# Optimization experiments

Measured on AMD Instinct MI355X. Metric: run time of the kernel, lower is better.

## Reference

```python
import jax, jax.numpy as jnp
import numpy as np

DIM = 128
NUM_TILES = 50000
NUM_PIECES = 25000
E_TT = 600000
E_PT = 400000


def _mean_aggregate(msgs, dst, num_dst):
    # msgs: [E, dim], dst: [E] int -> [num_dst, dim]
    agg = jax.ops.segment_sum(msgs, dst, num_segments=num_dst)
    cnt = jax.ops.segment_sum(jnp.ones((dst.shape[0], 1), msgs.dtype), dst,
                              num_segments=num_dst)
    return agg / jnp.maximum(cnt, 1.0)


def _linear(x, W, b):
    # torch nn.Linear: y = x @ W.T + b, W: [out, in]
    return x @ W.T + b


def setup_inputs() -> dict:
    key = jax.random.key(0)
    ks = jax.random.split(key, 20)
    s = 1.0 / np.sqrt(DIM)
    s2 = 1.0 / np.sqrt(2 * DIM)
    inp = {
        "tile_h": jax.random.normal(ks[0], (NUM_TILES, DIM), jnp.float32),
        "piece_h": jax.random.normal(ks[1], (NUM_PIECES, DIM), jnp.float32),
        "tile_src": jax.random.randint(ks[2], (E_PT,), 0, NUM_TILES),
        "piece_dst": jax.random.randint(ks[3], (E_PT,), 0, NUM_PIECES),
        "piece_src": jax.random.randint(ks[4], (E_PT,), 0, NUM_PIECES),
        "tile_dst": jax.random.randint(ks[5], (E_PT,), 0, NUM_TILES),
        "t_src": jax.random.randint(ks[6], (E_TT,), 0, NUM_TILES),
        "t_dst": jax.random.randint(ks[7], (E_TT,), 0, NUM_TILES),
        # weights: torch Linear layout [out_features, in_features]
        "W_t2p": jax.random.uniform(ks[8], (DIM, DIM), jnp.float32, -s, s),
        "b_t2p": jax.random.uniform(ks[9], (DIM,), jnp.float32, -s, s),
        "W_pu": jax.random.uniform(ks[10], (DIM, 2 * DIM), jnp.float32, -s2, s2),
        "b_pu": jax.random.uniform(ks[11], (DIM,), jnp.float32, -s2, s2),
        "W_p2t": jax.random.uniform(ks[12], (DIM, DIM), jnp.float32, -s, s),
        "b_p2t": jax.random.uniform(ks[13], (DIM,), jnp.float32, -s, s),
        "W_tup": jax.random.uniform(ks[14], (DIM, 2 * DIM), jnp.float32, -s2, s2),
        "b_tup": jax.random.uniform(ks[15], (DIM,), jnp.float32, -s2, s2),
        "W_t2t": jax.random.uniform(ks[16], (DIM, DIM), jnp.float32, -s, s),
        "b_t2t": jax.random.uniform(ks[17], (DIM,), jnp.float32, -s, s),
        "W_tut": jax.random.uniform(ks[18], (DIM, 2 * DIM), jnp.float32, -s2, s2),
        "b_tut": jax.random.uniform(ks[19], (DIM,), jnp.float32, -s2, s2),
    }
    return inp


def reference(tile_h, piece_h, tile_src, piece_dst, piece_src, tile_dst,
              t_src, t_dst,
              W_t2p, b_t2p, W_pu, b_pu, W_p2t, b_p2t,
              W_tup, b_tup, W_t2t, b_t2t, W_tut, b_tut):
    num_tiles = tile_h.shape[0]
    num_pieces = piece_h.shape[0]

    # Stage 1: tile -> piece
    msgs = _linear(tile_h[tile_src], W_t2p, b_t2p)          # [E_pt, dim]
    agg = _mean_aggregate(msgs, piece_dst, num_pieces)
    piece_h = jax.nn.relu(_linear(jnp.concatenate([piece_h, agg], axis=1), W_pu, b_pu))

    # Stage 2: piece -> tile
    msgs = _linear(piece_h[piece_src], W_p2t, b_p2t)        # [E_pt, dim]
    agg = _mean_aggregate(msgs, tile_dst, num_tiles)
    tile_h = jax.nn.relu(_linear(jnp.concatenate([tile_h, agg], axis=1), W_tup, b_tup))

    # Stage 3: tile -> tile
    msgs = _linear(tile_h[t_src], W_t2t, b_t2t)             # [E_tt, dim]
    agg = _mean_aggregate(msgs, t_dst, num_tiles)
    tile_h = jax.nn.relu(_linear(jnp.concatenate([tile_h, agg], axis=1), W_tut, b_tut))

    return (tile_h, piece_h)
```

## Files before the change

### kernel.cpp

```cpp
#include <hip/hip_runtime.h>
#include <hip/hip_bf16.h>

#define DIM 128
#define EPB 4096
#define BINS 512

typedef unsigned short u16;
typedef unsigned int u32;
typedef __attribute__((ext_vector_type(8))) short v8s;
typedef __attribute__((ext_vector_type(4))) float v4f;

__device__ __forceinline__ float bf2f(u16 u) {
    union { unsigned int i; float f; } v;
    v.i = ((unsigned int)u) << 16;
    return v.f;
}

__device__ __forceinline__ u16 f2bf(float f) {
    union { float f; unsigned int i; } v;
    v.f = f;
    unsigned int x = v.i;
    return (u16)((x + 0x7fffu + ((x >> 16) & 1u)) >> 16);
}

__device__ __forceinline__ uint4 pack8(float4 x0, float4 x1) {
    uint4 o;
    o.x = (u32)f2bf(x0.x) | ((u32)f2bf(x0.y) << 16);
    o.y = (u32)f2bf(x0.z) | ((u32)f2bf(x0.w) << 16);
    o.z = (u32)f2bf(x1.x) | ((u32)f2bf(x1.y) << 16);
    o.w = (u32)f2bf(x1.z) | ((u32)f2bf(x1.w) << 16);
    return o;
}

struct CvtArgs { const float* s[8]; u32 pfx[9]; };
__global__ __launch_bounds__(256) void cvt_all(CvtArgs a, u16* __restrict__ dst, int n8)
{
    int g = blockIdx.x * 256 + threadIdx.x;
    if (g >= n8) return;
    u32 flat = (u32)g * 8;
    int seg = 0;
    #pragma unroll
    for (int i = 1; i < 8; ++i) if (flat >= a.pfx[i]) seg = i;
    const float4* fp = (const float4*)(a.s[seg] + (flat - a.pfx[seg]));
    *(uint4*)(dst + flat) = pack8(fp[0], fp[1]);
}

__global__ __launch_bounds__(256) void rs_count(
    const int* __restrict__ piece_dst, const int* __restrict__ tile_dst,
    const int* __restrict__ t_dst, int EPT, int ETT,
    int* __restrict__ counts, int NBLK)
{
    __shared__ int h[BINS];
    const int t = threadIdx.x;
    for (int d = t; d < BINS; d += 256) h[d] = 0;
    __syncthreads();
    const int blk = blockIdx.x;
    const int ET = 2 * EPT + ETT;
    #pragma unroll
    for (int j = 0; j < EPB / 256; ++j) {
        int e = blk * EPB + j * 256 + t;
        if (e < ET) {
            int d;
            if (e < EPT)            d = (piece_dst[e] >> 9);
            else if (e < 2 * EPT)   d = 128 | (tile_dst[e - EPT] >> 9);
            else                    d = 256 | (t_dst[e - 2 * EPT] >> 9);
            atomicAdd(&h[d], 1);
        }
    }
    __syncthreads();
    for (int d = t; d < BINS; d += 256) counts[d * NBLK + blk] = h[d];
}

__global__ __launch_bounds__(256) void scan_gpart(const int* __restrict__ in,
                                                  int* __restrict__ out,
                                                  int* __restrict__ bsum, int n)
{
    __shared__ int ls[256];
    const int blk = blockIdx.x, t = threadIdx.x;
    const int base = blk * 2048;
    int v[8]; int s = 0;
    #pragma unroll
    for (int i = 0; i < 8; ++i) {
        int idx = base + t * 8 + i;
        v[i] = (idx < n) ? in[idx] : 0;
        s += v[i];
    }
    ls[t] = s;
    __syncthreads();
    #pragma unroll
    for (int o = 1; o < 256; o <<= 1) {
        int x = (t >= o) ? ls[t - o] : 0;
        __syncthreads();
        ls[t] += x;
        __syncthreads();
    }
    int run = (t == 0) ? 0 : ls[t - 1];
    #pragma unroll
    for (int i = 0; i < 8; ++i) {
        int idx = base + t * 8 + i;
        if (idx < n) out[idx] = run;
        run += v[i];
    }
    if (t == 255) bsum[blk] = ls[255];
}

__global__ __launch_bounds__(256) void scan_gfix(int* __restrict__ out,
                                                 const int* __restrict__ bsum, int n)
{
    __shared__ int off_s;
    const int blk = blockIdx.x, t = threadIdx.x;
    if (t == 0) {
        int o = 0;
        for (int i = 0; i < blk; ++i) o += bsum[i];
        off_s = o;
    }
    __syncthreads();
    const int off = off_s;
    const int base = blk * 2048;
    #pragma unroll
    for (int i = 0; i < 8; ++i) {
        int idx = base + t * 8 + i;
        if (idx < n) out[idx] += off;
    }
}

__global__ __launch_bounds__(256) void rs_scatter(
    const int* __restrict__ tile_src, const int* __restrict__ piece_dst,
    const int* __restrict__ piece_src, const int* __restrict__ tile_dst,
    const int* __restrict__ t_src, const int* __restrict__ t_dst,
    int EPT, int ETT,
    const int* __restrict__ countsS, int NBLK, int* __restrict__ T)
{
    __shared__ int p[BINS];
    const int t = threadIdx.x;
    const int blk = blockIdx.x;
    for (int d = t; d < BINS; d += 256) p[d] = countsS[d * NBLK + blk];
    __syncthreads();
    const int ET = 2 * EPT + ETT;
    #pragma unroll
    for (int j = 0; j < EPB / 256; ++j) {
        int e = blk * EPB + j * 256 + t;
        if (e < ET) {
            int dst, src, d;
            if (e < EPT) {
                dst = piece_dst[e]; src = tile_src[e]; d = dst >> 9;
            } else if (e < 2 * EPT) {
                int le = e - EPT;
                dst = tile_dst[le]; src = piece_src[le]; d = 128 | (dst >> 9);
            } else {
                int le = e - 2 * EPT;
                dst = t_dst[le]; src = t_src[le]; d = 256 | (dst >> 9);
            }
            int pos = atomicAdd(&p[d], 1);
            T[pos] = ((dst & 511) << 17) | src;
        }
    }
}

__global__ __launch_bounds__(256) void bucket_sort(
    const int* __restrict__ T, const int* __restrict__ countsS, int NBLK, int ET,
    int EPT, int ETT, int NP, int NT,
    int* __restrict__ el, int* __restrict__ rowptr)
{
    const int d = blockIdx.x;
    const int seg = d >> 7;
    if (seg > 2) return;
    const int dhi = d & 127;
    int Nseg, segOff, rb, Eseg;
    if (seg == 0)      { Nseg = NP; segOff = 0;       rb = 0;                 Eseg = EPT; }
    else if (seg == 1) { Nseg = NT; segOff = EPT;     rb = NP + 1;            Eseg = EPT; }
    else               { Nseg = NT; segOff = 2 * EPT; rb = NP + 1 + NT + 1;   Eseg = ETT; }

    const int bstart = countsS[d * NBLK];
    const int bend = (d < BINS - 1) ? countsS[(d + 1) * NBLK] : ET;

    __shared__ int hist[BINS];
    __shared__ int pos[BINS];
    __shared__ int ls[256];
    const int t = threadIdx.x;
    for (int i = t; i < BINS; i += 256) hist[i] = 0;
    __syncthreads();
    for (int j = bstart + t; j < bend; j += 256)
        atomicAdd(&hist[T[j] >> 17], 1);
    __syncthreads();
    int c0 = hist[2 * t], c1 = hist[2 * t + 1];
    ls[t] = c0 + c1;
    __syncthreads();
    #pragma unroll
    for (int o = 1; o < 256; o <<= 1) {
        int x = (t >= o) ? ls[t - o] : 0;
        __syncthreads();
        ls[t] += x;
        __syncthreads();
    }
    int ex = (t == 0) ? 0 : ls[t - 1];
    pos[2 * t]     = bstart + ex;
    pos[2 * t + 1] = bstart + ex + c0;
    __syncthreads();
    for (int i = t; i < BINS; i += 256) {
        int n = dhi * 512 + i;
        if (n < Nseg) rowptr[rb + n] = pos[i] - segOff;
    }
    if (t == 0 && dhi == ((Nseg - 1) >> 9)) rowptr[rb + Nseg] = Eseg;
    __syncthreads();
    for (int j = bstart + t; j < bend; j += 256) {
        int v = T[j];
        int p = atomicAdd(&pos[v >> 17], 1);
        el[p] = v & 0x1ffff;
    }
}

__global__ __launch_bounds__(256) void gather_mean_kernel(
    const u16* __restrict__ feat,
    const int* __restrict__ elist, const int* __restrict__ rowptr,
    int N, u16* __restrict__ meanA)
{
    int node = blockIdx.x * 8 + (threadIdx.x >> 5);
    int lane = threadIdx.x & 31;
    if (node >= N) return;
    int r0 = rowptr[node], r1 = rowptr[node + 1];
    float a0 = 0.f, a1 = 0.f, a2 = 0.f, a3 = 0.f;
    float b0 = 0.f, b1 = 0.f, b2 = 0.f, b3 = 0.f;
    int j = r0;
    for (; j + 4 <= r1; j += 4) {
        int s0 = elist[j], s1 = elist[j + 1], s2 = elist[j + 2], s3 = elist[j + 3];
        uint2 v0 = ((const uint2*)(feat + (size_t)s0 * DIM))[lane];
        uint2 v1 = ((const uint2*)(feat + (size_t)s1 * DIM))[lane];
        uint2 v2 = ((const uint2*)(feat + (size_t)s2 * DIM))[lane];
        uint2 v3 = ((const uint2*)(feat + (size_t)s3 * DIM))[lane];
        a0 += bf2f((u16)(v0.x & 0xffffu)); a1 += bf2f((u16)(v0.x >> 16));
        a2 += bf2f((u16)(v0.y & 0xffffu)); a3 += bf2f((u16)(v0.y >> 16));
        b0 += bf2f((u16)(v1.x & 0xffffu)); b1 += bf2f((u16)(v1.x >> 16));
        b2 += bf2f((u16)(v1.y & 0xffffu)); b3 += bf2f((u16)(v1.y >> 16));
        a0 += bf2f((u16)(v2.x & 0xffffu)); a1 += bf2f((u16)(v2.x >> 16));
        a2 += bf2f((u16)(v2.y & 0xffffu)); a3 += bf2f((u16)(v2.y >> 16));
        b0 += bf2f((u16)(v3.x & 0xffffu)); b1 += bf2f((u16)(v3.x >> 16));
        b2 += bf2f((u16)(v3.y & 0xffffu)); b3 += bf2f((u16)(v3.y >> 16));
    }
    for (; j < r1; ++j) {
        int s = elist[j];
        uint2 v = ((const uint2*)(feat + (size_t)s * DIM))[lane];
        a0 += bf2f((u16)(v.x & 0xffffu)); a1 += bf2f((u16)(v.x >> 16));
        a2 += bf2f((u16)(v.y & 0xffffu)); a3 += bf2f((u16)(v.y >> 16));
    }
    a0 += b0; a1 += b1; a2 += b2; a3 += b3;
    float sc = (r1 > r0) ? (1.f / (float)(r1 - r0)) : 0.f;
    uint2 o;
    o.x = (u32)f2bf(a0 * sc) | ((u32)f2bf(a1 * sc) << 16);
    o.y = (u32)f2bf(a2 * sc) | ((u32)f2bf(a3 * sc) << 16);
    ((uint2*)(meanA + (size_t)node * DIM))[lane] = o;
}

__global__ __launch_bounds__(256) void stage_fused(
    const u16* __restrict__ meanA, const int* __restrict__ rowptr,
    const u16* __restrict__ Wt, const float* __restrict__ bt,
    const u16* __restrict__ A1, const u16* __restrict__ Wu,
    const float* __restrict__ bu,
    u16* __restrict__ outC, float* __restrict__ outF, int N)
{
    __shared__ u16 Wl[128][136];
    __shared__ u16 Al[64][136];
    __shared__ u16 Bl[64][136];
    const int tid = threadIdx.x;
    const int nb = blockIdx.x * 64;
    const int wave = tid >> 6;
    const int lane = tid & 63;
    const int m = lane & 15;
    const int quad = lane >> 4;
    const int arow = wave * 16 + m;

    #pragma unroll
    for (int i = 0; i < 8; ++i) {
        int c = i * 256 + tid;
        int row = c >> 4;
        int c8 = (c & 15) * 8;
        *(uint4*)&Wl[row][c8] = *(const uint4*)(Wt + row * 128 + c8);
    }
    #pragma unroll
    for (int i = 0; i < 4; ++i) {
        int c = i * 256 + tid;
        int row = c >> 4;
        int c8 = (c & 15) * 8;
        int n = nb + row;
        uint4 v = {0u, 0u, 0u, 0u};
        if (n < N) v = *(const uint4*)(meanA + (size_t)n * DIM + c8);
        *(uint4*)&Al[row][c8] = v;
    }
    __syncthreads();

    v4f acct[8];
    #pragma unroll
    for (int t = 0; t < 8; ++t) acct[t] = (v4f){0.f, 0.f, 0.f, 0.f};
    #pragma unroll
    for (int k0 = 0; k0 < 128; k0 += 32) {
        v8s a = *(const v8s*)&Al[arow][k0 + quad * 8];
        #pragma unroll
        for (int t = 0; t < 8; ++t) {
            v8s b = *(const v8s*)&Wl[t * 16 + m][k0 + quad * 8];
            acct[t] = __builtin_amdgcn_mfma_f32_16x16x32_bf16(a, b, acct[t], 0, 0, 0);
        }
    }
    __syncthreads();

    {
        float btv[8];
        #pragma unroll
        for (int t = 0; t < 8; ++t) btv[t] = bt[t * 16 + m];
        #pragma unroll
        for (int r = 0; r < 4; ++r) {
            int n = nb + wave * 16 + quad * 4 + r;
            bool has = (n < N) && (rowptr[n + 1] > rowptr[n]);
            #pragma unroll
            for (int t = 0; t < 8; ++t) {
                float val = has ? (acct[t][r] + btv[t]) : 0.f;
                Bl[wave * 16 + quad * 4 + r][t * 16 + m] = f2bf(val);
            }
        }
    }
    #pragma unroll
    for (int i = 0; i < 8; ++i) {
        int c = i * 256 + tid;
        int row = c >> 4;
        int c8 = (c & 15) * 8;
        *(uint4*)&Wl[row][c8] = *(const uint4*)(Wu + row * 256 + c8);
    }
    #pragma unroll
    for (int i = 0; i < 4; ++i) {
        int c = i * 256 + tid;
        int row = c >> 4;
        int c8 = (c & 15) * 8;
        int n = nb + row;
        uint4 v = {0u, 0u, 0u, 0u};
        if (n < N) v = *(const uint4*)(A1 + (size_t)n * DIM + c8);
        *(uint4*)&Al[row][c8] = v;
    }
    __syncthreads();

    v4f accu[8];
    #pragma unroll
    for (int t = 0; t < 8; ++t) accu[t] = (v4f){0.f, 0.f, 0.f, 0.f};
    #pragma unroll
    for (int k0 = 0; k0 < 128; k0 += 32) {
        v8s a = *(const v8s*)&Al[arow][k0 + quad * 8];
        #pragma unroll
        for (int t = 0; t < 8; ++t) {
            v8s b = *(const v8s*)&Wl[t * 16 + m][k0 + quad * 8];
            accu[t] = __builtin_amdgcn_mfma_f32_16x16x32_bf16(a, b, accu[t], 0, 0, 0);
        }
    }
    __syncthreads();

    #pragma unroll
    for (int i = 0; i < 8; ++i) {
        int c = i * 256 + tid;
        int row = c >> 4;
        int c8 = (c & 15) * 8;
        *(uint4*)&Wl[row][c8] = *(const uint4*)(Wu + row * 256 + 128 + c8);
    }
    __syncthreads();

    #pragma unroll
    for (int k0 = 0; k0 < 128; k0 += 32) {
        v8s a = *(const v8s*)&Bl[arow][k0 + quad * 8];
        #pragma unroll
        for (int t = 0; t < 8; ++t) {
            v8s b = *(const v8s*)&Wl[t * 16 + m][k0 + quad * 8];
            accu[t] = __builtin_amdgcn_mfma_f32_16x16x32_bf16(a, b, accu[t], 0, 0, 0);
        }
    }

    float buv[8];
    #pragma unroll
    for (int t = 0; t < 8; ++t) buv[t] = bu[t * 16 + m];
    #pragma unroll
    for (int r = 0; r < 4; ++r) {
        int n = nb + wave * 16 + quad * 4 + r;
        if (n >= N) continue;
        #pragma unroll
        for (int t = 0; t < 8; ++t) {
            float val = accu[t][r] + buv[t];
            val = val > 0.f ? val : 0.f;
            if (outC) outC[(size_t)n * DIM + t * 16 + m] = f2bf(val);
            if (outF) outF[(size_t)n * DIM + t * 16 + m] = val;
        }
    }
}

extern "C" void kernel_launch(void* const* d_in, const int* in_sizes, int n_in,
                              void* d_out, int out_size, void* d_ws, size_t ws_size,
                              hipStream_t stream)
{
    const float* tile_h   = (const float*)d_in[0];
    const float* piece_h  = (const float*)d_in[1];
    const int* tile_src   = (const int*)d_in[2];
    const int* piece_dst  = (const int*)d_in[3];
    const int* piece_src  = (const int*)d_in[4];
    const int* tile_dst   = (const int*)d_in[5];
    const int* t_src      = (const int*)d_in[6];
    const int* t_dst      = (const int*)d_in[7];
    const float* b_t2p = (const float*)d_in[9];
    const float* b_pu  = (const float*)d_in[11];
    const float* b_p2t = (const float*)d_in[13];
    const float* b_tup = (const float*)d_in[15];
    const float* b_t2t = (const float*)d_in[17];
    const float* b_tut = (const float*)d_in[19];

    const int NT  = in_sizes[0] / DIM;
    const int NP  = in_sizes[1] / DIM;
    const int EPT = in_sizes[2];
    const int ETT = in_sizes[6];
    const int ET  = 2 * EPT + ETT;

    const int NBLK = (ET + EPB - 1) / EPB;
    const int n2 = BINS * NBLK;
    const int SB = (n2 + 2047) / 2048;

    char* ws = (char*)d_ws;
    size_t off = 0;
    int* counts = (int*)(ws + off);   off += (size_t)n2 * sizeof(int);
    off = (off + 255) & ~(size_t)255;
    int* countsS = (int*)(ws + off);  off += (size_t)n2 * sizeof(int);
    off = (off + 255) & ~(size_t)255;
    int* gbsum = (int*)(ws + off);    off += (size_t)((SB + 63) & ~63) * sizeof(int);
    off = (off + 255) & ~(size_t)255;
    int* rowptr = (int*)(ws + off);   off += (size_t)(NP + 2 * NT + 3) * sizeof(int);
    off = (off + 255) & ~(size_t)255;
    int* el = (int*)(ws + off);       off += (size_t)ET * sizeof(int);
    off = (off + 255) & ~(size_t)255;
    u16* A = (u16*)(ws + off);        off += (size_t)NT * DIM * sizeof(u16);
    off = (off + 255) & ~(size_t)255;
    u16* C = (u16*)(ws + off);        off += (size_t)NT * DIM * sizeof(u16);
    off = (off + 255) & ~(size_t)255;
    u16* arena = (u16*)(ws + off);

    int* T = (int*)A;

    const u32 nTh = (u32)NT * DIM, nPh = (u32)NP * DIM;
    u32 pfx[9];
    pfx[0] = 0;
    pfx[1] = nTh;
    pfx[2] = pfx[1] + nPh;
    pfx[3] = pfx[2] + 16384;
    pfx[4] = pfx[3] + 32768;
    pfx[5] = pfx[4] + 16384;
    pfx[6] = pfx[5] + 32768;
    pfx[7] = pfx[6] + 16384;
    pfx[8] = pfx[7] + 32768;

    u16* Th = arena + pfx[0];
    u16* Ph = arena + pfx[1];
    const u16* Wt2p = arena + pfx[2];
    const u16* Wpu  = arena + pfx[3];
    const u16* Wp2t = arena + pfx[4];
    const u16* Wtup = arena + pfx[5];
    const u16* Wt2t = arena + pfx[6];
    const u16* Wtut = arena + pfx[7];

    int* rp1 = rowptr;
    int* rp2 = rowptr + NP + 1;
    int* rp3 = rowptr + NP + 1 + NT + 1;
    int* el1 = el;
    int* el2 = el + EPT;
    int* el3 = el + 2 * EPT;

    float* out_tile  = (float*)d_out;
    float* out_piece = out_tile + (size_t)NT * DIM;

    dim3 blk(256);
    dim3 g_rs((unsigned)NBLK);
    dim3 g_scan((unsigned)SB);
    dim3 g_bs((unsigned)BINS);
    dim3 g_gp((unsigned)((NP + 7) / 8));
    dim3 g_gt((unsigned)((NT + 7) / 8));
    dim3 g_np((unsigned)((NP + 63) / 64));
    dim3 g_nt((unsigned)((NT + 63) / 64));

    CvtArgs ca;
    ca.s[0] = tile_h; ca.s[1] = piece_h;
    ca.s[2] = (const float*)d_in[8];  ca.s[3] = (const float*)d_in[10];
    ca.s[4] = (const float*)d_in[12]; ca.s[5] = (const float*)d_in[14];
    ca.s[6] = (const float*)d_in[16]; ca.s[7] = (const float*)d_in[18];
    for (int i = 0; i < 9; ++i) ca.pfx[i] = pfx[i];
    int n8 = (int)(pfx[8] / 8);
    hipLaunchKernelGGL(cvt_all, dim3((n8 + 255) / 256), blk, 0, stream, ca, arena, n8);

    hipLaunchKernelGGL(rs_count, g_rs, blk, 0, stream,
                       piece_dst, tile_dst, t_dst, EPT, ETT, counts, NBLK);
    hipLaunchKernelGGL(scan_gpart, g_scan, blk, 0, stream, counts, countsS, gbsum, n2);
    hipLaunchKernelGGL(scan_gfix, g_scan, blk, 0, stream, countsS, gbsum, n2);
    hipLaunchKernelGGL(rs_scatter, g_rs, blk, 0, stream,
                       tile_src, piece_dst, piece_src, tile_dst, t_src, t_dst,
                       EPT, ETT, countsS, NBLK, T);
    hipLaunchKernelGGL(bucket_sort, g_bs, blk, 0, stream,
                       T, countsS, NBLK, ET, EPT, ETT, NP, NT, el, rowptr);

    hipLaunchKernelGGL(gather_mean_kernel, g_gp, blk, 0, stream,
                       Th, el1, rp1, NP, A);
    hipLaunchKernelGGL(stage_fused, g_np, blk, 0, stream,
                       A, rp1, Wt2p, b_t2p, Ph, Wpu, b_pu, C, out_piece, NP);

    hipLaunchKernelGGL(gather_mean_kernel, g_gt, blk, 0, stream,
                       C, el2, rp2, NT, A);
    hipLaunchKernelGGL(stage_fused, g_nt, blk, 0, stream,
                       A, rp2, Wp2t, b_p2t, Th, Wtup, b_tup, C, (float*)nullptr, NT);

    hipLaunchKernelGGL(gather_mean_kernel, g_gt, blk, 0, stream,
                       C, el3, rp3, NT, A);
    hipLaunchKernelGGL(stage_fused, g_nt, blk, 0, stream,
                       A, rp3, Wt2t, b_t2t, C, Wtut, b_tut, (u16*)nullptr, out_tile, NT);
}
```

Before: 312.1 us.

## Fuse conversion with radix count, enlarge edge blocks, widen gather loads

Merges the fp32-to-bf16 conversion kernel and the bucket-count kernel into one launch, with a block-index split between the two roles. Raises edges per block from 4096 to 16384, which shrinks the counts array and the scan, with partial unrolling. The gather-mean kernel now uses 16 lanes per node with 16-byte loads instead of 32 lanes with 8-byte loads. The aim is fewer launches, less scan work and fewer memory transactions per row, at the cost of less parallelism in the scatter and sort phases.

After: 349.9 us. +12.1%, slower.

```diff
diff --git a/kernel.cpp b/kernel.cpp
--- a/kernel.cpp
+++ b/kernel.cpp
@@ -2,7 +2,7 @@
 #include <hip/hip_bf16.h>
 
 #define DIM 128
-#define EPB 4096
+#define EPB 16384
 #define BINS 512
 
 typedef unsigned short u16;
@@ -33,30 +33,30 @@
 }
 
 struct CvtArgs { const float* s[8]; u32 pfx[9]; };
-__global__ __launch_bounds__(256) void cvt_all(CvtArgs a, u16* __restrict__ dst, int n8)
-{
-    int g = blockIdx.x * 256 + threadIdx.x;
-    if (g >= n8) return;
-    u32 flat = (u32)g * 8;
-    int seg = 0;
-    #pragma unroll
-    for (int i = 1; i < 8; ++i) if (flat >= a.pfx[i]) seg = i;
-    const float4* fp = (const float4*)(a.s[seg] + (flat - a.pfx[seg]));
-    *(uint4*)(dst + flat) = pack8(fp[0], fp[1]);
-}
-
-__global__ __launch_bounds__(256) void rs_count(
+__global__ __launch_bounds__(256) void cvt_and_count(
+    CvtArgs a, u16* __restrict__ dst, int n8, int cvtB,
     const int* __restrict__ piece_dst, const int* __restrict__ tile_dst,
     const int* __restrict__ t_dst, int EPT, int ETT,
     int* __restrict__ counts, int NBLK)
 {
     __shared__ int h[BINS];
     const int t = threadIdx.x;
+    if (blockIdx.x < cvtB) {
+        int g = blockIdx.x * 256 + t;
+        if (g >= n8) return;
+        u32 flat = (u32)g * 8;
+        int seg = 0;
+        #pragma unroll
+        for (int i = 1; i < 8; ++i) if (flat >= a.pfx[i]) seg = i;
+        const float4* fp = (const float4*)(a.s[seg] + (flat - a.pfx[seg]));
+        *(uint4*)(dst + flat) = pack8(fp[0], fp[1]);
+        return;
+    }
+    const int blk = blockIdx.x - cvtB;
     for (int d = t; d < BINS; d += 256) h[d] = 0;
     __syncthreads();
-    const int blk = blockIdx.x;
     const int ET = 2 * EPT + ETT;
-    #pragma unroll
+    #pragma unroll 4
     for (int j = 0; j < EPB / 256; ++j) {
         int e = blk * EPB + j * 256 + t;
         if (e < ET) {
@@ -137,7 +137,7 @@
     for (int d = t; d < BINS; d += 256) p[d] = countsS[d * NBLK + blk];
     __syncthreads();
     const int ET = 2 * EPT + ETT;
-    #pragma unroll
+    #pragma unroll 4
     for (int j = 0; j < EPB / 256; ++j) {
         int e = blk * EPB + j * 256 + t;
         if (e < ET) {
@@ -215,40 +215,51 @@
     const int* __restrict__ elist, const int* __restrict__ rowptr,
     int N, u16* __restrict__ meanA)
 {
-    int node = blockIdx.x * 8 + (threadIdx.x >> 5);
-    int lane = threadIdx.x & 31;
+    int node = blockIdx.x * 16 + (threadIdx.x >> 4);
+    int lane = threadIdx.x & 15;
     if (node >= N) return;
     int r0 = rowptr[node], r1 = rowptr[node + 1];
     float a0 = 0.f, a1 = 0.f, a2 = 0.f, a3 = 0.f;
-    float b0 = 0.f, b1 = 0.f, b2 = 0.f, b3 = 0.f;
+    float a4 = 0.f, a5 = 0.f, a6 = 0.f, a7 = 0.f;
     int j = r0;
     for (; j + 4 <= r1; j += 4) {
         int s0 = elist[j], s1 = elist[j + 1], s2 = elist[j + 2], s3 = elist[j + 3];
-        uint2 v0 = ((const uint2*)(feat + (size_t)s0 * DIM))[lane];
-        uint2 v1 = ((const uint2*)(feat + (size_t)s1 * DIM))[lane];
-        uint2 v2 = ((const uint2*)(feat + (size_t)s2 * DIM))[lane];
-        uint2 v3 = ((const uint2*)(feat + (size_t)s3 * DIM))[lane];
+        uint4 v0 = ((const uint4*)(feat + (size_t)s0 * DIM))[lane];
+        uint4 v1 = ((const uint4*)(feat + (size_t)s1 * DIM))[lane];
+        uint4 v2 = ((const uint4*)(feat + (size_t)s2 * DIM))[lane];
+        uint4 v3 = ((const uint4*)(feat + (size_t)s3 * DIM))[lane];
         a0 += bf2f((u16)(v0.x & 0xffffu)); a1 += bf2f((u16)(v0.x >> 16));
         a2 += bf2f((u16)(v0.y & 0xffffu)); a3 += bf2f((u16)(v0.y >> 16));
-        b0 += bf2f((u16)(v1.x & 0xffffu)); b1 += bf2f((u16)(v1.x >> 16));
-        b2 += bf2f((u16)(v1.y & 0xffffu)); b3 += bf2f((u16)(v1.y >> 16));
+        a4 += bf2f((u16)(v0.z & 0xffffu)); a5 += bf2f((u16)(v0.z >> 16));
+        a6 += bf2f((u16)(v0.w & 0xffffu)); a7 += bf2f((u16)(v0.w >> 16));
+        a0 += bf2f((u16)(v1.x & 0xffffu)); a1 += bf2f((u16)(v1.x >> 16));
+        a2 += bf2f((u16)(v1.y & 0xffffu)); a3 += bf2f((u16)(v1.y >> 16));
+        a4 += bf2f((u16)(v1.z & 0xffffu)); a5 += bf2f((u16)(v1.z >> 16));
+        a6 += bf2f((u16)(v1.w & 0xffffu)); a7 += bf2f((u16)(v1.w >> 16));
         a0 += bf2f((u16)(v2.x & 0xffffu)); a1 += bf2f((u16)(v2.x >> 16));
         a2 += bf2f((u16)(v2.y & 0xffffu)); a3 += bf2f((u16)(v2.y >> 16));
-        b0 += bf2f((u16)(v3.x & 0xffffu)); b1 += bf2f((u16)(v3.x >> 16));
-        b2 += bf2f((u16)(v3.y & 0xffffu)); b3 += bf2f((u16)(v3.y >> 16));
+        a4 += bf2f((u16)(v2.z & 0xffffu)); a5 += bf2f((u16)(v2.z >> 16));
+        a6 += bf2f((u16)(v2.w & 0xffffu)); a7 += bf2f((u16)(v2.w >> 16));
+        a0 += bf2f((u16)(v3.x & 0xffffu)); a1 += bf2f((u16)(v3.x >> 16));
+        a2 += bf2f((u16)(v3.y & 0xffffu)); a3 += bf2f((u16)(v3.y >> 16));
+        a4 += bf2f((u16)(v3.z & 0xffffu)); a5 += bf2f((u16)(v3.z >> 16));
+        a6 += bf2f((u16)(v3.w & 0xffffu)); a7 += bf2f((u16)(v3.w >> 16));
     }
     for (; j < r1; ++j) {
         int s = elist[j];
-        uint2 v = ((const uint2*)(feat + (size_t)s * DIM))[lane];
+        uint4 v = ((const uint4*)(feat + (size_t)s * DIM))[lane];
         a0 += bf2f((u16)(v.x & 0xffffu)); a1 += bf2f((u16)(v.x >> 16));
         a2 += bf2f((u16)(v.y & 0xffffu)); a3 += bf2f((u16)(v.y >> 16));
-    }
-    a0 += b0; a1 += b1; a2 += b2; a3 += b3;
+        a4 += bf2f((u16)(v.z & 0xffffu)); a5 += bf2f((u16)(v.z >> 16));
+        a6 += bf2f((u16)(v.w & 0xffffu)); a7 += bf2f((u16)(v.w >> 16));
+    }
     float sc = (r1 > r0) ? (1.f / (float)(r1 - r0)) : 0.f;
-    uint2 o;
+    uint4 o;
     o.x = (u32)f2bf(a0 * sc) | ((u32)f2bf(a1 * sc) << 16);
     o.y = (u32)f2bf(a2 * sc) | ((u32)f2bf(a3 * sc) << 16);
-    ((uint2*)(meanA + (size_t)node * DIM))[lane] = o;
+    o.z = (u32)f2bf(a4 * sc) | ((u32)f2bf(a5 * sc) << 16);
+    o.w = (u32)f2bf(a6 * sc) | ((u32)f2bf(a7 * sc) << 16);
+    ((uint4*)(meanA + (size_t)node * DIM))[lane] = o;
 }
 
 __global__ __launch_bounds__(256) void stage_fused(
@@ -467,11 +478,14 @@
     float* out_piece = out_tile + (size_t)NT * DIM;
 
     dim3 blk(256);
+    int n8 = (int)(pfx[8] / 8);
+    const int cvtB = (n8 + 255) / 256;
+    dim3 g_fat((unsigned)(cvtB + NBLK));
     dim3 g_rs((unsigned)NBLK);
     dim3 g_scan((unsigned)SB);
     dim3 g_bs((unsigned)BINS);
-    dim3 g_gp((unsigned)((NP + 7) / 8));
-    dim3 g_gt((unsigned)((NT + 7) / 8));
+    dim3 g_gp((unsigned)((NP + 15) / 16));
+    dim3 g_gt((unsigned)((NT + 15) / 16));
     dim3 g_np((unsigned)((NP + 63) / 64));
     dim3 g_nt((unsigned)((NT + 63) / 64));
 
@@ -481,11 +495,10 @@
     ca.s[4] = (const float*)d_in[12]; ca.s[5] = (const float*)d_in[14];
     ca.s[6] = (const float*)d_in[16]; ca.s[7] = (const float*)d_in[18];
     for (int i = 0; i < 9; ++i) ca.pfx[i] = pfx[i];
-    int n8 = (int)(pfx[8] / 8);
-    hipLaunchKernelGGL(cvt_all, dim3((n8 + 255) / 256), blk, 0, stream, ca, arena, n8);
-
-    hipLaunchKernelGGL(rs_count, g_rs, blk, 0, stream,
+    hipLaunchKernelGGL(cvt_and_count, g_fat, blk, 0, stream,
+                       ca, arena, n8, cvtB,
                        piece_dst, tile_dst, t_dst, EPT, ETT, counts, NBLK);
+
     hipLaunchKernelGGL(scan_gpart, g_scan, blk, 0, stream, counts, countsS, gbsum, n2);
     hipLaunchKernelGGL(scan_gfix, g_scan, blk, 0, stream, countsS, gbsum, n2);
     hipLaunchKernelGGL(rs_scatter, g_rs, blk, 0, stream,
```
